# Kernel optimization log

Hardware: AMD Instinct MI355X
Metric: run time of the kernel (lower is better)

## Reference

```python
import jax, jax.numpy as jnp
import numpy as np

NUM_HEADS = 16
EMBED = 1024
HEAD_DIM = EMBED // NUM_HEADS


def setup_inputs() -> dict:
    key = jax.random.key(0)
    k1, k2, k3, k4, k5 = jax.random.split(key, 5)
    B, N, D = 16, 1024, EMBED
    s_in = 1.0 / np.sqrt(D)
    x = jax.random.normal(k1, (B, N, D), dtype=jnp.float32)
    # Linear weights stored as [in, out] so y = x @ W + b (equiv to torch x @ W.T + b)
    W_qkv = jax.random.uniform(k2, (D, 3 * D), dtype=jnp.float32, minval=-s_in, maxval=s_in)
    b_qkv = jax.random.uniform(k3, (3 * D,), dtype=jnp.float32, minval=-s_in, maxval=s_in)
    W_fc = jax.random.uniform(k4, (D, D), dtype=jnp.float32, minval=-s_in, maxval=s_in)
    b_fc = jax.random.uniform(k5, (D,), dtype=jnp.float32, minval=-s_in, maxval=s_in)
    return {"x": x, "W_qkv": W_qkv, "b_qkv": b_qkv, "W_fc": W_fc, "b_fc": b_fc}


def reference(x, W_qkv, b_qkv, W_fc, b_fc):
    B, N, D = x.shape
    H, d_k = NUM_HEADS, HEAD_DIM
    qkv = x @ W_qkv + b_qkv                      # [B, N, 3D]
    qkv = qkv.reshape(B, N, 3, H, d_k)
    qkv = jnp.transpose(qkv, (2, 0, 3, 1, 4))    # [3, B, H, N, d_k]
    Q, K, V = qkv[0], qkv[1], qkv[2]
    scale = 1.0 / jnp.sqrt(jnp.asarray(d_k, dtype=x.dtype))
    scores = jnp.einsum("bhqd,bhkd->bhqk", Q, K) * scale
    attn = jax.nn.softmax(scores, axis=-1)       # dropout is identity in eval mode
    context = jnp.einsum("bhqk,bhkd->bhqd", attn, V)
    context = jnp.transpose(context, (0, 2, 1, 3)).reshape(B, N, D)
    return context @ W_fc + b_fc
```

## Files before the change

### kernel.cpp

```cpp
#include <hip/hip_runtime.h>
#include <cstdint>
#include <cstddef>

typedef unsigned short u16;
typedef __bf16 bf16_t;
typedef bf16_t bf16x8 __attribute__((ext_vector_type(8)));
typedef float f32x4 __attribute__((ext_vector_type(4)));

#define MFMA16(a, b, c) __builtin_amdgcn_mfma_f32_16x16x32_bf16((a), (b), (c), 0, 0, 0)
#define GLOBAL_AS __attribute__((address_space(1)))
#define LDS_AS __attribute__((address_space(3)))

#define SOFT_M 8.0f

__device__ __forceinline__ u16 f2bf(float f) {
    unsigned u = __float_as_uint(f);
    u += 0x7FFFu + ((u >> 16) & 1u);
    return (u16)(u >> 16);
}
__device__ __forceinline__ u16 f2bf_trunc(float f) {
    return (u16)(__float_as_uint(f) >> 16);
}
__device__ __forceinline__ void gll16(const u16* g, u16* l) {
    __builtin_amdgcn_global_load_lds((const GLOBAL_AS unsigned int*)g,
                                     (LDS_AS unsigned int*)l, 16, 0, 0);
}

__global__ __launch_bounds__(256) void conv_x_kernel(const float* __restrict__ x,
                                                     u16* __restrict__ xb) {
    int i = blockIdx.x * 256 + threadIdx.x;
    float4 v = ((const float4*)x)[i];
    ushort4 o;
    o.x = f2bf(v.x); o.y = f2bf(v.y); o.z = f2bf(v.z); o.w = f2bf(v.w);
    ((ushort4*)xb)[i] = o;
}

__global__ __launch_bounds__(256) void transpose_w_kernel(const float* __restrict__ W,
                                                          u16* __restrict__ Wt,
                                                          int R, int C) {
    __shared__ u16 tile[32][33];
    int c0 = blockIdx.x * 32, r0 = blockIdx.y * 32;
    int tx = threadIdx.x, ty = threadIdx.y;
#pragma unroll
    for (int i = 0; i < 4; i++)
        tile[ty + i * 8][tx] = f2bf(W[(size_t)(r0 + ty + i * 8) * C + c0 + tx]);
    __syncthreads();
#pragma unroll
    for (int i = 0; i < 4; i++)
        Wt[(size_t)(c0 + ty + i * 8) * R + r0 + tx] = tile[tx][ty + i * 8];
}

__global__ __launch_bounds__(256) void gemm_qkv_kernel(const u16* __restrict__ A,
                                                       const u16* __restrict__ Bt,
                                                       const float* __restrict__ bias,
                                                       u16* __restrict__ Qb,
                                                       u16* __restrict__ Kb,
                                                       u16* __restrict__ Vt) {
    const int K = 1024;
    __shared__ u16 As[128 * 32];
    __shared__ u16 Bs[128 * 32];
    int t = threadIdx.x;
    int m0 = blockIdx.x * 128, n0 = blockIdx.y * 128;
    int lane = t & 63, wid = t >> 6;
    int lr = lane & 15, quad = lane >> 4;
    int wm = (wid >> 1) * 64, wn = (wid & 1) * 64;
    int srow = lane >> 2, scol = (lane & 3) * 8;

    f32x4 acc[4][4];
    f32x4 zf = {0.f, 0.f, 0.f, 0.f};
#pragma unroll
    for (int i = 0; i < 4; i++)
#pragma unroll
        for (int j = 0; j < 4; j++) acc[i][j] = zf;

    for (int k0 = 0; k0 < K; k0 += 32) {
        __syncthreads();
#pragma unroll
        for (int i = 0; i < 2; i++) {
            int c = wid * 2 + i;
            int row = c * 16 + srow;
            gll16(A + (size_t)(m0 + row) * K + k0 + scol, &As[c * 512]);
            gll16(Bt + (size_t)(n0 + row) * K + k0 + scol, &Bs[c * 512]);
        }
        __syncthreads();
        bf16x8 af[4], bfr[4];
#pragma unroll
        for (int mt = 0; mt < 4; mt++)
            af[mt] = *(const bf16x8*)&As[(wm + mt * 16 + lr) * 32 + quad * 8];
#pragma unroll
        for (int nt = 0; nt < 4; nt++)
            bfr[nt] = *(const bf16x8*)&Bs[(wn + nt * 16 + lr) * 32 + quad * 8];
#pragma unroll
        for (int mt = 0; mt < 4; mt++)
#pragma unroll
            for (int nt = 0; nt < 4; nt++)
                acc[mt][nt] = MFMA16(af[mt], bfr[nt], acc[mt][nt]);
    }

    int s = n0 >> 10;
    if (s == 2) {
#pragma unroll
        for (int nt = 0; nt < 4; nt++) {
            int col = n0 + wn + nt * 16 + lr;
            int h = (col >> 6) & 15, d = col & 63;
            float bv = bias[col];
            int dsw = (d & 7) << 3;
#pragma unroll
            for (int mt = 0; mt < 4; mt++) {
                f32x4 v = acc[mt][nt];
                int mb = m0 + wm + mt * 16 + quad * 4;
                int bb = mb >> 10, nn = mb & 1023;
                int nn2 = (nn & ~63) | ((nn & 63) ^ dsw);
                ushort4 o;
                o.x = f2bf(v[0] + bv); o.y = f2bf(v[1] + bv);
                o.z = f2bf(v[2] + bv); o.w = f2bf(v[3] + bv);
                *(ushort4*)&Vt[(((size_t)(bb * 16 + h)) * 64 + d) * 1024 + nn2] = o;
            }
        }
    } else {
        u16* dst = (s == 0) ? Qb : Kb;
        float scale = (s == 0) ? 0.125f * 1.44269504089f : 1.0f;
#pragma unroll
        for (int nt = 0; nt < 4; nt++) {
            int col = n0 + wn + nt * 16 + lr;
            int h = (col >> 6) & 15, d = col & 63;
            float bv = bias[col];
#pragma unroll
            for (int mt = 0; mt < 4; mt++) {
                f32x4 v = acc[mt][nt];
#pragma unroll
                for (int r = 0; r < 4; r++) {
                    int m = m0 + wm + mt * 16 + quad * 4 + r;
                    int bb = m >> 10, nn = m & 1023;
                    int d2 = (s == 1) ? (d ^ ((nn & 7) << 3)) : d;
                    dst[(((size_t)(bb * 16 + h)) * 1024 + nn) * 64 + d2] =
                        f2bf((v[r] + bv) * scale);
                }
            }
        }
    }
}

__device__ __forceinline__ uint4 build_pa(f32x4 s0, f32x4 s1, float& lacc, bool qodd) {
    unsigned w[4];
    float part = 0.f;
#pragma unroll
    for (int half = 0; half < 2; half++) {
        unsigned lo = f2bf_trunc(__builtin_amdgcn_exp2f(s0[half * 2] - SOFT_M));
        unsigned hi = f2bf_trunc(__builtin_amdgcn_exp2f(s0[half * 2 + 1] - SOFT_M));
        part += __uint_as_float(lo << 16) + __uint_as_float(hi << 16);
        w[half] = lo | (hi << 16);
    }
#pragma unroll
    for (int half = 0; half < 2; half++) {
        unsigned lo = f2bf_trunc(__builtin_amdgcn_exp2f(s1[half * 2] - SOFT_M));
        unsigned hi = f2bf_trunc(__builtin_amdgcn_exp2f(s1[half * 2 + 1] - SOFT_M));
        part += __uint_as_float(lo << 16) + __uint_as_float(hi << 16);
        w[2 + half] = lo | (hi << 16);
    }
    lacc += part;
    unsigned x0 = qodd ? w[0] : w[2];
    unsigned x1 = qodd ? w[1] : w[3];
    unsigned y0 = __shfl_xor(x0, 16);
    unsigned y1 = __shfl_xor(x1, 16);
    uint4 r;
    r.x = qodd ? y0 : w[0];
    r.y = qodd ? y1 : w[1];
    r.z = qodd ? w[2] : y0;
    r.w = qodd ? w[3] : y1;
    return r;
}

__global__ __launch_bounds__(256, 4) void flash_attn_kernel(const u16* __restrict__ Qb,
                                                            const u16* __restrict__ Kb,
                                                            const u16* __restrict__ Vt,
                                                            u16* __restrict__ ctx) {
    __shared__ u16 smem[16384];
    u16* Ks0 = smem;
    u16* Vs0 = smem + 8192;
    int t = threadIdx.x, lane = t & 63, wid = t >> 6;
    int lr = lane & 15, quad = lane >> 4;
    int bh = blockIdx.x, q0 = blockIdx.y * 128;
    int b = bh >> 4, h = bh & 15;
    int xsw = (lr & 7) << 3;

    const u16* Kg = Kb + (size_t)bh * 65536;
    const u16* Vg = Vt + (size_t)bh * 65536;

#pragma unroll
    for (int i = 0; i < 2; i++) {
        gll16(Kg + wid * 1024 + i * 512 + lane * 8, Ks0 + wid * 1024 + i * 512);
        int row = wid * 16 + i * 8 + (lane >> 3);
        gll16(Vg + (size_t)row * 1024 + (lane & 7) * 8, Vs0 + wid * 1024 + i * 512);
    }

    const u16* Qw = Qb + ((size_t)bh * 1024 + q0 + wid * 32) * 64;
    bf16x8 qf[2][2];
#pragma unroll
    for (int mt = 0; mt < 2; mt++)
#pragma unroll
        for (int kk = 0; kk < 2; kk++)
            qf[mt][kk] = *(const bf16x8*)(Qw + (mt * 16 + lr) * 64 + kk * 32 + quad * 8);

    f32x4 oacc[2][4];
    f32x4 zf = {0.f, 0.f, 0.f, 0.f};
#pragma unroll
    for (int mt = 0; mt < 2; mt++)
#pragma unroll
        for (int dt = 0; dt < 4; dt++) oacc[mt][dt] = zf;
    float lsum0 = 0.f, lsum1 = 0.f;
    bool qodd = (quad & 1) != 0;
    int vperm8 = (((quad & 1) << 1) | (quad >> 1)) * 8;

    __syncthreads();

    for (int kt = 0; kt < 16; kt++) {
        int cur = kt & 1;
        if (kt < 15) {
            u16* kd = Ks0 + (cur ^ 1) * 4096;
            u16* vd = Vs0 + (cur ^ 1) * 4096;
            const u16* ks = Kg + (size_t)(kt + 1) * 4096;
#pragma unroll
            for (int i = 0; i < 2; i++) {
                gll16(ks + wid * 1024 + i * 512 + lane * 8, kd + wid * 1024 + i * 512);
                int row = wid * 16 + i * 8 + (lane >> 3);
                gll16(Vg + (size_t)row * 1024 + (kt + 1) * 64 + (lane & 7) * 8,
                      vd + wid * 1024 + i * 512);
            }
        }

        const u16* Kc = Ks0 + cur * 4096;
        f32x4 sc[2][4];
#pragma unroll
        for (int mt = 0; mt < 2; mt++)
#pragma unroll
            for (int nt = 0; nt < 4; nt++) sc[mt][nt] = zf;
#pragma unroll
        for (int nt = 0; nt < 4; nt++) {
            bf16x8 kf0 = *(const bf16x8*)&Kc[(nt * 16 + lr) * 64 + ((quad * 8) ^ xsw)];
            bf16x8 kf1 = *(const bf16x8*)&Kc[(nt * 16 + lr) * 64 + ((quad * 8 + 32) ^ xsw)];
#pragma unroll
            for (int mt = 0; mt < 2; mt++) {
                sc[mt][nt] = MFMA16(kf0, qf[mt][0], sc[mt][nt]);
                sc[mt][nt] = MFMA16(kf1, qf[mt][1], sc[mt][nt]);
            }
        }

        const u16* Vc = Vs0 + cur * 4096;
#pragma unroll
        for (int kc = 0; kc < 2; kc++) {
            uint4 pw0 = build_pa(sc[0][kc * 2], sc[0][kc * 2 + 1], lsum0, qodd);
            uint4 pw1 = build_pa(sc[1][kc * 2], sc[1][kc * 2 + 1], lsum1, qodd);
            bf16x8 pa0 = *(const bf16x8*)&pw0;
            bf16x8 pa1 = *(const bf16x8*)&pw1;
#pragma unroll
            for (int dt = 0; dt < 4; dt++) {
                bf16x8 vv = *(const bf16x8*)&Vc[(dt * 16 + lr) * 64 +
                                                ((kc * 32 + vperm8) ^ xsw)];
                oacc[0][dt] = MFMA16(pa0, vv, oacc[0][dt]);
                oacc[1][dt] = MFMA16(pa1, vv, oacc[1][dt]);
            }
        }

        __syncthreads();
    }

    u16* Ow = smem + wid * 2304;
#pragma unroll
    for (int mt = 0; mt < 2; mt++) {
        float lf = (mt == 0) ? lsum0 : lsum1;
        lf += __shfl_xor(lf, 16);
        lf += __shfl_xor(lf, 32);
        float inv = 1.0f / lf;
#pragma unroll
        for (int r = 0; r < 4; r++) {
            float invr = __shfl(inv, (lane & 48) | (quad * 4 + r));
#pragma unroll
            for (int dt = 0; dt < 4; dt++)
                Ow[(mt * 16 + quad * 4 + r) * 72 + dt * 16 + lr] =
                    f2bf(oacc[mt][dt][r] * invr);
        }
    }
#pragma unroll
    for (int j = 0; j < 4; j++) {
        int r2 = j * 8 + (lane >> 3);
        uint4 ov = *(const uint4*)&Ow[r2 * 72 + (lane & 7) * 8];
        int row = q0 + wid * 32 + r2;
        *(uint4*)&ctx[((size_t)b * 1024 + row) * 1024 + h * 64 + (lane & 7) * 8] = ov;
    }
}

__global__ __launch_bounds__(256) void gemm_proj_kernel(const u16* __restrict__ A,
                                                        const u16* __restrict__ Bt,
                                                        const float* __restrict__ bias,
                                                        float* __restrict__ out) {
    const int K = 1024;
    __shared__ u16 As[128 * 32];
    __shared__ u16 Bs[128 * 32];
    int t = threadIdx.x;
    int m0 = blockIdx.x * 128, n0 = blockIdx.y * 128;
    int lane = t & 63, wid = t >> 6;
    int lr = lane & 15, quad = lane >> 4;
    int wm = (wid >> 1) * 64, wn = (wid & 1) * 64;
    int srow = lane >> 2, scol = (lane & 3) * 8;

    f32x4 acc[4][4];
    f32x4 zf = {0.f, 0.f, 0.f, 0.f};
#pragma unroll
    for (int i = 0; i < 4; i++)
#pragma unroll
        for (int j = 0; j < 4; j++) acc[i][j] = zf;

    for (int k0 = 0; k0 < K; k0 += 32) {
        __syncthreads();
#pragma unroll
        for (int i = 0; i < 2; i++) {
            int c = wid * 2 + i;
            int row = c * 16 + srow;
            gll16(A + (size_t)(m0 + row) * K + k0 + scol, &As[c * 512]);
            gll16(Bt + (size_t)(n0 + row) * K + k0 + scol, &Bs[c * 512]);
        }
        __syncthreads();
        bf16x8 af[4], bfr[4];
#pragma unroll
        for (int mt = 0; mt < 4; mt++)
            af[mt] = *(const bf16x8*)&As[(wm + mt * 16 + lr) * 32 + quad * 8];
#pragma unroll
        for (int nt = 0; nt < 4; nt++)
            bfr[nt] = *(const bf16x8*)&Bs[(wn + nt * 16 + lr) * 32 + quad * 8];
#pragma unroll
        for (int mt = 0; mt < 4; mt++)
#pragma unroll
            for (int nt = 0; nt < 4; nt++)
                acc[mt][nt] = MFMA16(af[mt], bfr[nt], acc[mt][nt]);
    }

#pragma unroll
    for (int nt = 0; nt < 4; nt++) {
        int col = n0 + wn + nt * 16 + lr;
        float bv = bias[col];
#pragma unroll
        for (int mt = 0; mt < 4; mt++) {
            f32x4 v = acc[mt][nt];
#pragma unroll
            for (int r = 0; r < 4; r++) {
                int m = m0 + wm + mt * 16 + quad * 4 + r;
                out[(size_t)m * 1024 + col] = v[r] + bv;
            }
        }
    }
}

extern "C" void kernel_launch(void* const* d_in, const int* in_sizes, int n_in,
                              void* d_out, int out_size, void* d_ws, size_t ws_size,
                              hipStream_t stream) {
    const float* x     = (const float*)d_in[0];
    const float* W_qkv = (const float*)d_in[1];
    const float* b_qkv = (const float*)d_in[2];
    const float* W_fc  = (const float*)d_in[3];
    const float* b_fc  = (const float*)d_in[4];
    float* out = (float*)d_out;
    char* ws = (char*)d_ws;

    u16* xb  = (u16*)(ws + 0);
    u16* wqt = (u16*)(ws + 33554432);
    u16* wft = (u16*)(ws + 39845888);
    u16* Qb  = (u16*)(ws + 41943040);
    u16* Kb  = (u16*)(ws + 75497472);
    u16* Vt  = (u16*)(ws + 109051904);
    u16* ctx = (u16*)(ws + 0);

    conv_x_kernel<<<16384, 256, 0, stream>>>(x, xb);
    transpose_w_kernel<<<dim3(96, 32), dim3(32, 8), 0, stream>>>(W_qkv, wqt, 1024, 3072);
    transpose_w_kernel<<<dim3(32, 32), dim3(32, 8), 0, stream>>>(W_fc, wft, 1024, 1024);
    gemm_qkv_kernel<<<dim3(128, 24), 256, 0, stream>>>(xb, wqt, b_qkv, Qb, Kb, Vt);
    flash_attn_kernel<<<dim3(256, 8), 256, 0, stream>>>(Qb, Kb, Vt, ctx);
    gemm_proj_kernel<<<dim3(128, 8), 256, 0, stream>>>(ctx, wft, b_fc, out);
}
```

Baseline: 428.8 us.

## Replace QKV and projection GEMMs with pipelined 256x256 tile kernel

Both GEMMs now use a single templated kernel with 256x256 tiles, 512 threads, a 4-stage LDS ring filled by direct global-to-LDS loads two k-steps ahead, XOR-swizzled LDS layout, and split MFMA phases with s_setprio. The aim is more data reuse per tile, fewer LDS bank conflicts, and overlap of global loads with MFMA work instead of sync-load-compute per k-step. In exchange it uses 128KB of LDS and many more accumulator registers per block, and the grid has far fewer blocks (768 and 256), so occupancy and wave-quantization on the GPU may suffer.

```diff
diff --git a/kernel.cpp b/kernel.cpp
--- a/kernel.cpp
+++ b/kernel.cpp
@@ -50,91 +50,150 @@
         Wt[(size_t)(c0 + ty + i * 8) * R + r0 + tx] = tile[tx][ty + i * 8];
 }
 
-__global__ __launch_bounds__(256) void gemm_qkv_kernel(const u16* __restrict__ A,
-                                                       const u16* __restrict__ Bt,
-                                                       const float* __restrict__ bias,
-                                                       u16* __restrict__ Qb,
-                                                       u16* __restrict__ Kb,
-                                                       u16* __restrict__ Vt) {
-    const int K = 1024;
-    __shared__ u16 As[128 * 32];
-    __shared__ u16 Bs[128 * 32];
+template <bool PROJ>
+__global__ __launch_bounds__(512, 2) void gemm256_kernel(const u16* __restrict__ A,
+                                                         const u16* __restrict__ Bt,
+                                                         const float* __restrict__ bias,
+                                                         u16* __restrict__ Qb,
+                                                         u16* __restrict__ Kb,
+                                                         u16* __restrict__ Vt,
+                                                         float* __restrict__ outF) {
+    __shared__ u16 lds[65536];
+    u16* ldsA = lds;
+    u16* ldsB = lds + 32768;
+
     int t = threadIdx.x;
-    int m0 = blockIdx.x * 128, n0 = blockIdx.y * 128;
     int lane = t & 63, wid = t >> 6;
     int lr = lane & 15, quad = lane >> 4;
-    int wm = (wid >> 1) * 64, wn = (wid & 1) * 64;
-    int srow = lane >> 2, scol = (lane & 3) * 8;
-
-    f32x4 acc[4][4];
+    int m0 = blockIdx.x * 256, n0 = blockIdx.y * 256;
+    int wmBase = (wid >> 2) * 128;
+    int wnBase = (wid & 3) * 64;
+    int kcol = (quad * 8) ^ (((lr >> 1) & 3) << 3);
+
+    int srow = wid * 16 + (lane >> 2);
+    int schk = ((lane & 3) ^ ((lane >> 3) & 3)) * 8;
+    const u16* AgT = A + (size_t)(m0 + srow) * 1024 + schk;
+    const u16* BgT = Bt + (size_t)(n0 + srow) * 1024 + schk;
+    int dstOff = wid * 512;
+
+    auto stageA = [&](int tt) {
+        u16* d = ldsA + (tt & 3) * 8192 + dstOff;
+        const u16* s = AgT + (size_t)tt * 32;
+        gll16(s, d);
+        gll16(s + 131072, d + 4096);
+    };
+    auto stageB = [&](int tt) {
+        u16* d = ldsB + (tt & 3) * 8192 + dstOff;
+        const u16* s = BgT + (size_t)tt * 32;
+        gll16(s, d);
+        gll16(s + 131072, d + 4096);
+    };
+
+    f32x4 acc[8][4];
     f32x4 zf = {0.f, 0.f, 0.f, 0.f};
 #pragma unroll
-    for (int i = 0; i < 4; i++)
+    for (int i = 0; i < 8; i++)
 #pragma unroll
         for (int j = 0; j < 4; j++) acc[i][j] = zf;
 
-    for (int k0 = 0; k0 < K; k0 += 32) {
-        __syncthreads();
-#pragma unroll
-        for (int i = 0; i < 2; i++) {
-            int c = wid * 2 + i;
-            int row = c * 16 + srow;
-            gll16(A + (size_t)(m0 + row) * K + k0 + scol, &As[c * 512]);
-            gll16(Bt + (size_t)(n0 + row) * K + k0 + scol, &Bs[c * 512]);
-        }
-        __syncthreads();
-        bf16x8 af[4], bfr[4];
-#pragma unroll
-        for (int mt = 0; mt < 4; mt++)
-            af[mt] = *(const bf16x8*)&As[(wm + mt * 16 + lr) * 32 + quad * 8];
-#pragma unroll
-        for (int nt = 0; nt < 4; nt++)
-            bfr[nt] = *(const bf16x8*)&Bs[(wn + nt * 16 + lr) * 32 + quad * 8];
-#pragma unroll
-        for (int mt = 0; mt < 4; mt++)
-#pragma unroll
-            for (int nt = 0; nt < 4; nt++)
-                acc[mt][nt] = MFMA16(af[mt], bfr[nt], acc[mt][nt]);
-    }
-
-    int s = n0 >> 10;
-    if (s == 2) {
+    stageA(0); stageB(0);
+    stageA(1); stageB(1);
+    asm volatile("s_waitcnt vmcnt(4)" ::: "memory");
+    __builtin_amdgcn_s_barrier();
+    __builtin_amdgcn_sched_barrier(0);
+
+#pragma unroll 1
+    for (int kt = 0; kt < 32; ++kt) {
+        const u16* SA = ldsA + (kt & 3) * 8192;
+        const u16* SB = ldsB + (kt & 3) * 8192;
+        bf16x8 af[8];
+#pragma unroll
+        for (int mt = 0; mt < 8; mt++)
+            af[mt] = *(const bf16x8*)&SA[(wmBase + mt * 16 + lr) * 32 + kcol];
+        bf16x8 b0 = *(const bf16x8*)&SB[(wnBase + lr) * 32 + kcol];
+        bf16x8 b1 = *(const bf16x8*)&SB[(wnBase + 16 + lr) * 32 + kcol];
+        if (kt < 30) stageA(kt + 2);
+        __builtin_amdgcn_s_barrier();
+        __builtin_amdgcn_s_setprio(1);
+#pragma unroll
+        for (int mt = 0; mt < 8; mt++) {
+            acc[mt][0] = MFMA16(af[mt], b0, acc[mt][0]);
+            acc[mt][1] = MFMA16(af[mt], b1, acc[mt][1]);
+        }
+        __builtin_amdgcn_s_setprio(0);
+        __builtin_amdgcn_s_barrier();
+        bf16x8 b2 = *(const bf16x8*)&SB[(wnBase + 32 + lr) * 32 + kcol];
+        bf16x8 b3 = *(const bf16x8*)&SB[(wnBase + 48 + lr) * 32 + kcol];
+        if (kt < 30) stageB(kt + 2);
+        __builtin_amdgcn_s_barrier();
+        __builtin_amdgcn_s_setprio(1);
+#pragma unroll
+        for (int mt = 0; mt < 8; mt++) {
+            acc[mt][2] = MFMA16(af[mt], b2, acc[mt][2]);
+            acc[mt][3] = MFMA16(af[mt], b3, acc[mt][3]);
+        }
+        __builtin_amdgcn_s_setprio(0);
+        if (kt <= 29)      asm volatile("s_waitcnt vmcnt(4)" ::: "memory");
+        else if (kt == 30) asm volatile("s_waitcnt vmcnt(0)" ::: "memory");
+        __builtin_amdgcn_s_barrier();
+        __builtin_amdgcn_sched_barrier(0);
+    }
+
+    if constexpr (PROJ) {
 #pragma unroll
         for (int nt = 0; nt < 4; nt++) {
-            int col = n0 + wn + nt * 16 + lr;
-            int h = (col >> 6) & 15, d = col & 63;
+            int col = n0 + wnBase + nt * 16 + lr;
             float bv = bias[col];
-            int dsw = (d & 7) << 3;
-#pragma unroll
-            for (int mt = 0; mt < 4; mt++) {
+#pragma unroll
+            for (int mt = 0; mt < 8; mt++) {
                 f32x4 v = acc[mt][nt];
-                int mb = m0 + wm + mt * 16 + quad * 4;
-                int bb = mb >> 10, nn = mb & 1023;
-                int nn2 = (nn & ~63) | ((nn & 63) ^ dsw);
-                ushort4 o;
-                o.x = f2bf(v[0] + bv); o.y = f2bf(v[1] + bv);
-                o.z = f2bf(v[2] + bv); o.w = f2bf(v[3] + bv);
-                *(ushort4*)&Vt[(((size_t)(bb * 16 + h)) * 64 + d) * 1024 + nn2] = o;
+#pragma unroll
+                for (int r = 0; r < 4; r++) {
+                    int m = m0 + wmBase + mt * 16 + quad * 4 + r;
+                    outF[(size_t)m * 1024 + col] = v[r] + bv;
+                }
             }
         }
     } else {
-        u16* dst = (s == 0) ? Qb : Kb;
-        float scale = (s == 0) ? 0.125f * 1.44269504089f : 1.0f;
-#pragma unroll
-        for (int nt = 0; nt < 4; nt++) {
-            int col = n0 + wn + nt * 16 + lr;
-            int h = (col >> 6) & 15, d = col & 63;
-            float bv = bias[col];
-#pragma unroll
-            for (int mt = 0; mt < 4; mt++) {
-                f32x4 v = acc[mt][nt];
-#pragma unroll
-                for (int r = 0; r < 4; r++) {
-                    int m = m0 + wm + mt * 16 + quad * 4 + r;
-                    int bb = m >> 10, nn = m & 1023;
-                    int d2 = (s == 1) ? (d ^ ((nn & 7) << 3)) : d;
-                    dst[(((size_t)(bb * 16 + h)) * 1024 + nn) * 64 + d2] =
-                        f2bf((v[r] + bv) * scale);
+        int s = n0 >> 10;
+        if (s == 2) {
+#pragma unroll
+            for (int nt = 0; nt < 4; nt++) {
+                int col = n0 + wnBase + nt * 16 + lr;
+                int h = (col >> 6) & 15, d = col & 63;
+                float bv = bias[col];
+                int dsw = (d & 7) << 3;
+#pragma unroll
+                for (int mt = 0; mt < 8; mt++) {
+                    f32x4 v = acc[mt][nt];
+                    int mb = m0 + wmBase + mt * 16 + quad * 4;
+                    int bb = mb >> 10, nn = mb & 1023;
+                    int nn2 = (nn & ~63) | ((nn & 63) ^ dsw);
+                    ushort4 o;
+                    o.x = f2bf(v[0] + bv); o.y = f2bf(v[1] + bv);
+                    o.z = f2bf(v[2] + bv); o.w = f2bf(v[3] + bv);
+                    *(ushort4*)&Vt[(((size_t)(bb * 16 + h)) * 64 + d) * 1024 + nn2] = o;
+                }
+            }
+        } else {
+            u16* dst = (s == 0) ? Qb : Kb;
+            float scale = (s == 0) ? 0.125f * 1.44269504089f : 1.0f;
+#pragma unroll
+            for (int nt = 0; nt < 4; nt++) {
+                int col = n0 + wnBase + nt * 16 + lr;
+                int h = (col >> 6) & 15, d = col & 63;
+                float bv = bias[col];
+#pragma unroll
+                for (int mt = 0; mt < 8; mt++) {
+                    f32x4 v = acc[mt][nt];
+#pragma unroll
+                    for (int r = 0; r < 4; r++) {
+                        int m = m0 + wmBase + mt * 16 + quad * 4 + r;
+                        int bb = m >> 10, nn = m & 1023;
+                        int d2 = (s == 1) ? (d ^ ((nn & 7) << 3)) : d;
+                        dst[(((size_t)(bb * 16 + h)) * 1024 + nn) * 64 + d2] =
+                            f2bf((v[r] + bv) * scale);
+                    }
                 }
             }
         }
@@ -290,67 +349,6 @@
     }
 }
 
-__global__ __launch_bounds__(256) void gemm_proj_kernel(const u16* __restrict__ A,
-                                                        const u16* __restrict__ Bt,
-                                                        const float* __restrict__ bias,
-                                                        float* __restrict__ out) {
-    const int K = 1024;
-    __shared__ u16 As[128 * 32];
-    __shared__ u16 Bs[128 * 32];
-    int t = threadIdx.x;
-    int m0 = blockIdx.x * 128, n0 = blockIdx.y * 128;
-    int lane = t & 63, wid = t >> 6;
-    int lr = lane & 15, quad = lane >> 4;
-    int wm = (wid >> 1) * 64, wn = (wid & 1) * 64;
-    int srow = lane >> 2, scol = (lane & 3) * 8;
-
-    f32x4 acc[4][4];
-    f32x4 zf = {0.f, 0.f, 0.f, 0.f};
-#pragma unroll
-    for (int i = 0; i < 4; i++)
-#pragma unroll
-        for (int j = 0; j < 4; j++) acc[i][j] = zf;
-
-    for (int k0 = 0; k0 < K; k0 += 32) {
-        __syncthreads();
-#pragma unroll
-        for (int i = 0; i < 2; i++) {
-            int c = wid * 2 + i;
-            int row = c * 16 + srow;
-            gll16(A + (size_t)(m0 + row) * K + k0 + scol, &As[c * 512]);
-            gll16(Bt + (size_t)(n0 + row) * K + k0 + scol, &Bs[c * 512]);
-        }
-        __syncthreads();
-        bf16x8 af[4], bfr[4];
-#pragma unroll
-        for (int mt = 0; mt < 4; mt++)
-            af[mt] = *(const bf16x8*)&As[(wm + mt * 16 + lr) * 32 + quad * 8];
-#pragma unroll
-        for (int nt = 0; nt < 4; nt++)
-            bfr[nt] = *(const bf16x8*)&Bs[(wn + nt * 16 + lr) * 32 + quad * 8];
-#pragma unroll
-        for (int mt = 0; mt < 4; mt++)
-#pragma unroll
-            for (int nt = 0; nt < 4; nt++)
-                acc[mt][nt] = MFMA16(af[mt], bfr[nt], acc[mt][nt]);
-    }
-
-#pragma unroll
-    for (int nt = 0; nt < 4; nt++) {
-        int col = n0 + wn + nt * 16 + lr;
-        float bv = bias[col];
-#pragma unroll
-        for (int mt = 0; mt < 4; mt++) {
-            f32x4 v = acc[mt][nt];
-#pragma unroll
-            for (int r = 0; r < 4; r++) {
-                int m = m0 + wm + mt * 16 + quad * 4 + r;
-                out[(size_t)m * 1024 + col] = v[r] + bv;
-            }
-        }
-    }
-}
-
 extern "C" void kernel_launch(void* const* d_in, const int* in_sizes, int n_in,
                               void* d_out, int out_size, void* d_ws, size_t ws_size,
                               hipStream_t stream) {
@@ -373,7 +371,9 @@
     conv_x_kernel<<<16384, 256, 0, stream>>>(x, xb);
     transpose_w_kernel<<<dim3(96, 32), dim3(32, 8), 0, stream>>>(W_qkv, wqt, 1024, 3072);
     transpose_w_kernel<<<dim3(32, 32), dim3(32, 8), 0, stream>>>(W_fc, wft, 1024, 1024);
-    gemm_qkv_kernel<<<dim3(128, 24), 256, 0, stream>>>(xb, wqt, b_qkv, Qb, Kb, Vt);
+    gemm256_kernel<false><<<dim3(64, 12), 512, 0, stream>>>(xb, wqt, b_qkv,
+                                                            Qb, Kb, Vt, nullptr);
     flash_attn_kernel<<<dim3(256, 8), 256, 0, stream>>>(Qb, Kb, Vt, ctx);
-    gemm_proj_kernel<<<dim3(128, 8), 256, 0, stream>>>(ctx, wft, b_fc, out);
-}
+    gemm256_kernel<true><<<dim3(64, 4), 512, 0, stream>>>(ctx, wft, b_fc,
+                                                          nullptr, nullptr, nullptr, out);
+}
```

New measurement: 391.4 us. -8.7%, faster.
